# Optimization experiments

Measured on AMD Instinct MI355X. Metric: run time of the kernel, lower is better.

Reference implementation:

```python
import jax, jax.numpy as jnp
import numpy as np

TOKENS, D_IN, D_OUT = 8192, 4096, 4096

def setup_inputs() -> dict:
    key = jax.random.key(0)
    k1, k2, k3 = jax.random.split(key, 3)
    x = jax.random.normal(k1, (TOKENS, D_IN), dtype=jnp.float32)
    # original init: uniform(-1, 1) on weights of shape [out, in]
    w_pos = jax.random.uniform(k2, (D_OUT, D_IN), dtype=jnp.float32, minval=-1.0, maxval=1.0)
    w_neg = jax.random.uniform(k3, (D_OUT, D_IN), dtype=jnp.float32, minval=-1.0, maxval=1.0)
    return {"x": x, "w_pos": w_pos, "w_neg": w_neg}

def _ste_binarize(w):
    # (w > 0).float() in fwd, identity grad (STE): stop_grad(bin - w) + w
    b = (w > 0).astype(w.dtype)
    return jax.lax.stop_gradient(b - w) + w

def reference(x, w_pos, w_neg):
    tern_pos = _ste_binarize(w_pos)  # [O, I]
    tern_neg = _ste_binarize(w_neg)  # [O, I]
    # y = x @ tern_pos^T - x @ tern_neg^T  (biases unused in original forward)
    y = jnp.einsum('ti,oi->to', x, tern_pos) - jnp.einsum('ti,oi->to', x, tern_neg)
    return y
```

## Files before the change

kernel.cpp:

```cpp
#include <hip/hip_runtime.h>
#include <stdint.h>


#define TOKENS 8192
#define DIN    4096
#define DOUT   4096

typedef __bf16  bf16x8  __attribute__((ext_vector_type(8)));
typedef float   floatx4 __attribute__((ext_vector_type(4)));

__device__ __forceinline__ void async_copy16(const void* g, void* l) {
  __builtin_amdgcn_global_load_lds(
      (const __attribute__((address_space(1))) void*)g,
      (__attribute__((address_space(3))) void*)l, 16, 0, 0);
}

__device__ __forceinline__ unsigned short f2bf_rne(float f) {
  union { float f; uint32_t u; } v; v.f = f;
  uint32_t u = v.u;
  u += 0x7fffu + ((u >> 16) & 1u);
  return (unsigned short)(u >> 16);
}

__device__ __forceinline__ unsigned short tern_bits(float p, float n) {
  bool bp = p > 0.0f, bn = n > 0.0f;
  return (unsigned short)(bp == bn ? 0u : (bp ? 0x3f80u : 0xbf80u));
}

__global__ __launch_bounds__(256) void prep_kernel(
    const float4* __restrict__ x, ushort4* __restrict__ xb,
    const float4* __restrict__ wp, const float4* __restrict__ wn,
    ushort4* __restrict__ t) {
  const uint32_t bid = blockIdx.x;
  if (bid < 8192u) {
    const uint32_t stride = 8192u * 256u;
    uint32_t i = bid * 256u + threadIdx.x;
#pragma unroll
    for (int it = 0; it < 4; ++it, i += stride) {
      float4 v = x[i];
      ushort4 o;
      o.x = f2bf_rne(v.x); o.y = f2bf_rne(v.y);
      o.z = f2bf_rne(v.z); o.w = f2bf_rne(v.w);
      xb[i] = o;
    }
  } else {
    const uint32_t stride = 4096u * 256u;
    uint32_t i = (bid - 8192u) * 256u + threadIdx.x;
#pragma unroll
    for (int it = 0; it < 4; ++it, i += stride) {
      float4 p = wp[i];
      float4 n = wn[i];
      ushort4 o;
      o.x = tern_bits(p.x, n.x);
      o.y = tern_bits(p.y, n.y);
      o.z = tern_bits(p.z, n.z);
      o.w = tern_bits(p.w, n.w);
      t[i] = o;
    }
  }
}


#define LDS_BUF   65536u
#define LDS_B_OFF 32768u
#define LDS_KC    16384u

__global__ __launch_bounds__(512, 2) void gemm_bt(
    const unsigned short* __restrict__ A,
    const unsigned short* __restrict__ B,
    float* __restrict__ C)
{
  __shared__ __align__(16) char lds[131072];

  const int tid   = threadIdx.x;
  const int lane  = tid & 63;
  const int wid   = tid >> 6;
  const int waveM = wid >> 2;
  const int waveN = wid & 3;

  const uint32_t flat = blockIdx.x;
  const uint32_t swz  = ((flat & 7u) << 6) | (flat >> 3);
  const uint32_t bm = (swz >> 4) * 256u;
  const uint32_t bn = (swz & 15u) * 256u;

  const uint32_t srow  = (uint32_t)(tid >> 6) * 32u + (uint32_t)((tid & 63) >> 2);
  const uint32_t slot  = (uint32_t)(tid & 3);
  const uint32_t chnk  = slot ^ ((srow >> 1) & 3u);
  const uint32_t stA   = (bm + srow) * (DIN * 2u) + chnk * 16u;
  const uint32_t stB   = (bn + srow) * (DIN * 2u) + chnk * 16u;
  const uint32_t ldsSt = (uint32_t)(tid >> 6) * 2048u + (uint32_t)(tid & 63) * 16u;
  const char* Ab = (const char*)A;
  const char* Bb = (const char*)B;

  const int mrow = lane & 15;
  const int q    = lane >> 4;
  const int xs   = (q ^ ((mrow >> 1) & 3)) * 16;
  const uint32_t aFragBase = (uint32_t)waveM * 8192u + (uint32_t)mrow * 64u + (uint32_t)xs;
  const uint32_t bFragBase = LDS_B_OFF + (uint32_t)waveN * 4096u
                           + (uint32_t)mrow * 64u + (uint32_t)xs;

  floatx4 acc[8][4];
#pragma unroll
  for (int m = 0; m < 8; ++m)
#pragma unroll
    for (int n = 0; n < 4; ++n)
      acc[m][n] = (floatx4)0.0f;

  bf16x8 a0[4], a1[4], b0[4], b1[4];

#define STAGE_A(BUF, KH, KB) do {                                          \
    uint32_t g_ = stA + (KB) + (KH) * 64u;                                 \
    uint32_t l_ = (BUF) * LDS_BUF + (KH) * LDS_KC + ldsSt;                 \
    async_copy16(Ab + g_,           lds + l_);                             \
    async_copy16(Ab + g_ + 131072u, lds + l_ + 1024u);                     \
  } while (0)

#define STAGE_B(BUF, KH, KB) do {                                          \
    uint32_t g_ = stB + (KB) + (KH) * 64u;                                 \
    uint32_t l_ = (BUF) * LDS_BUF + LDS_B_OFF + (KH) * LDS_KC + ldsSt;     \
    async_copy16(Bb + g_,           lds + l_);                             \
    async_copy16(Bb + g_ + 131072u, lds + l_ + 1024u);                     \
  } while (0)

#define IA(DST, BUF, KC, MH) do {                                          \
    _Pragma("unroll")                                                      \
    for (int m_ = 0; m_ < 4; ++m_)                                         \
      DST[m_] = *(const bf16x8*)(lds + (BUF) * LDS_BUF + (KC) * LDS_KC     \
                                 + (uint32_t)(m_ + (MH) * 4) * 1024u       \
                                 + aFragBase);                             \
  } while (0)

#define IB(DST, BUF, KC) do {                                              \
    _Pragma("unroll")                                                      \
    for (int n_ = 0; n_ < 4; ++n_)                                         \
      DST[n_] = *(const bf16x8*)(lds + (BUF) * LDS_BUF + (KC) * LDS_KC     \
                                 + (uint32_t)n_ * 1024u + bFragBase);      \
  } while (0)

#define VM8 asm volatile("s_waitcnt vmcnt(8)" ::: "memory")
#define NOPW ((void)0)

#define PHASE(MH, AV, BV, ISSUE_STMT, STAGE_STMT, VMW) do {                \
    asm volatile("s_waitcnt lgkmcnt(0)" ::: "memory");                     \
    __builtin_amdgcn_sched_barrier(0);                                     \
    ISSUE_STMT;                                                            \
    __builtin_amdgcn_sched_barrier(0);                                     \
    __builtin_amdgcn_s_setprio(1);                                         \
    _Pragma("unroll")                                                      \
    for (int m_ = 0; m_ < 4; ++m_)                                         \
      _Pragma("unroll")                                                    \
      for (int n_ = 0; n_ < 4; ++n_)                                       \
        acc[(MH) * 4 + m_][n_] = __builtin_amdgcn_mfma_f32_16x16x32_bf16(  \
            AV[m_], BV[n_], acc[(MH) * 4 + m_][n_], 0, 0, 0);              \
    __builtin_amdgcn_s_setprio(0);                                         \
    STAGE_STMT;                                                            \
    VMW;                                                                   \
    __builtin_amdgcn_s_barrier();                                          \
  } while (0)

  STAGE_B(0, 0, 0u);   STAGE_A(0, 0, 0u);
  STAGE_B(0, 1, 0u);   STAGE_A(0, 1, 0u);
  STAGE_B(1, 0, 128u); STAGE_A(1, 0, 128u);
  STAGE_B(1, 1, 128u);
  asm volatile("s_waitcnt vmcnt(10)" ::: "memory");
  __builtin_amdgcn_s_barrier();
  IB(b0, 0, 0); IA(a0, 0, 0, 0);

#pragma unroll 1
  for (int i = 0; i < 32; ++i) {
    const uint32_t kb1 = (uint32_t)(2 * i + 1) * 128u;
    const uint32_t kb2 = (uint32_t)((2 * i + 2) & 63) * 128u;
    const uint32_t kb3 = (uint32_t)((2 * i + 3) & 63) * 128u;

    PHASE(0, a0, b0, IA(a1, 0, 0, 1),                  STAGE_A(1, 1, kb1), VM8);
    PHASE(1, a1, b0, { IB(b1, 0, 1); IA(a0, 0, 1, 0); }, STAGE_B(0, 0, kb2), NOPW);
    PHASE(0, a0, b1, IA(a1, 0, 1, 1),                  STAGE_A(0, 0, kb2), VM8);
    PHASE(1, a1, b1, { IB(b0, 1, 0); IA(a0, 1, 0, 0); }, STAGE_B(0, 1, kb2), NOPW);
    PHASE(0, a0, b0, IA(a1, 1, 0, 1),                  STAGE_A(0, 1, kb2), VM8);
    PHASE(1, a1, b0, { IB(b1, 1, 1); IA(a0, 1, 1, 0); }, STAGE_B(1, 0, kb3), NOPW);
    PHASE(0, a0, b1, IA(a1, 1, 1, 1),                  STAGE_A(1, 0, kb3), VM8);
    PHASE(1, a1, b1, { IB(b0, 0, 0); IA(a0, 0, 0, 0); }, STAGE_B(1, 1, kb3), NOPW);
  }

  const int col0 = (int)bn + waveN * 64 + (lane & 15);
  const int row0 = (int)bm + waveM * 128 + (lane >> 4) * 4;
  float* Cp = C + (size_t)row0 * DOUT + col0;
#pragma unroll
  for (int m = 0; m < 8; ++m)
#pragma unroll
    for (int n = 0; n < 4; ++n)
#pragma unroll
      for (int r = 0; r < 4; ++r)
        Cp[(size_t)(m * 16 + r) * DOUT + n * 16] = acc[m][n][r];

#undef STAGE_A
#undef STAGE_B
#undef IA
#undef IB
#undef VM8
#undef NOPW
#undef PHASE
}

extern "C" void kernel_launch(void* const* d_in, const int* in_sizes, int n_in,
                              void* d_out, int out_size, void* d_ws, size_t ws_size,
                              hipStream_t stream) {
  const float* x  = (const float*)d_in[0];
  const float* wp = (const float*)d_in[1];
  const float* wn = (const float*)d_in[2];
  float* out = (float*)d_out;

  unsigned short* xb   = (unsigned short*)d_ws;
  unsigned short* tern = xb + (size_t)TOKENS * DIN;

  prep_kernel<<<12288, 256, 0, stream>>>(
      (const float4*)x, (ushort4*)xb,
      (const float4*)wp, (const float4*)wn, (ushort4*)tern);

  gemm_bt<<<TOKENS / 256 * (DOUT / 256), 512, 0, stream>>>(xb, tern, out);
}
```

Baseline: 537.7 us.

## Use inline-asm LDS reads with immediate offsets and split B-fragment loads across phases

Replaces the compiler-generated LDS fragment loads with inline ds_read_b128 instructions that use precomputed base addresses and immediate offsets, to cut address arithmetic. B-fragment loads are now spread evenly across phases (two per phase) instead of four at once, and every phase waits on vmcnt(8) instead of alternating phases. This balances LDS traffic and shortens per-phase issue bursts, but the tighter vmcnt waits and the asm volatile reads can stall or limit scheduler freedom. The prologue also issues redundant B reads.

Result: no change. 537.1 us (-0.1%).

```diff
diff --git a/kernel.cpp b/kernel.cpp
--- a/kernel.cpp
+++ b/kernel.cpp
@@ -95,9 +95,15 @@
   const int mrow = lane & 15;
   const int q    = lane >> 4;
   const int xs   = (q ^ ((mrow >> 1) & 3)) * 16;
+  const uint32_t ldsBase =
+      (uint32_t)(uintptr_t)(__attribute__((address_space(3))) char*)lds;
   const uint32_t aFragBase = (uint32_t)waveM * 8192u + (uint32_t)mrow * 64u + (uint32_t)xs;
   const uint32_t bFragBase = LDS_B_OFF + (uint32_t)waveN * 4096u
                            + (uint32_t)mrow * 64u + (uint32_t)xs;
+  const uint32_t aA0 = ldsBase + aFragBase;
+  const uint32_t aA1 = aA0 + LDS_BUF;
+  const uint32_t bA0 = ldsBase + bFragBase;
+  const uint32_t bA1 = bA0 + LDS_BUF;
 
   floatx4 acc[8][4];
 #pragma unroll
@@ -106,7 +112,23 @@
     for (int n = 0; n < 4; ++n)
       acc[m][n] = (floatx4)0.0f;
 
-  bf16x8 a0[4], a1[4], b0[4], b1[4];
+  floatx4 a0f[4], a1f[4], b0f[4], b1f[4];
+
+#define DSR(DST, ADDR, IMM)                                                \
+  asm volatile("ds_read_b128 %0, %1 offset:%c2"                            \
+               : "=v"(DST) : "v"(ADDR), "i"(IMM))
+
+#define IA4(DST, ADDR, KC, MH) do {                                        \
+    DSR(DST[0], ADDR, (KC) * 16384 + ((MH) * 4 + 0) * 1024);               \
+    DSR(DST[1], ADDR, (KC) * 16384 + ((MH) * 4 + 1) * 1024);               \
+    DSR(DST[2], ADDR, (KC) * 16384 + ((MH) * 4 + 2) * 1024);               \
+    DSR(DST[3], ADDR, (KC) * 16384 + ((MH) * 4 + 3) * 1024);               \
+  } while (0)
+
+#define IB2(DST, N0, ADDR, KC) do {                                        \
+    DSR(DST[N0],     ADDR, (KC) * 16384 + ((N0)) * 1024);                  \
+    DSR(DST[N0 + 1], ADDR, (KC) * 16384 + ((N0) + 1) * 1024);              \
+  } while (0)
 
 #define STAGE_A(BUF, KH, KB) do {                                          \
     uint32_t g_ = stA + (KB) + (KH) * 64u;                                 \
@@ -122,26 +144,9 @@
     async_copy16(Bb + g_ + 131072u, lds + l_ + 1024u);                     \
   } while (0)
 
-#define IA(DST, BUF, KC, MH) do {                                          \
-    _Pragma("unroll")                                                      \
-    for (int m_ = 0; m_ < 4; ++m_)                                         \
-      DST[m_] = *(const bf16x8*)(lds + (BUF) * LDS_BUF + (KC) * LDS_KC     \
-                                 + (uint32_t)(m_ + (MH) * 4) * 1024u       \
-                                 + aFragBase);                             \
-  } while (0)
-
-#define IB(DST, BUF, KC) do {                                              \
-    _Pragma("unroll")                                                      \
-    for (int n_ = 0; n_ < 4; ++n_)                                         \
-      DST[n_] = *(const bf16x8*)(lds + (BUF) * LDS_BUF + (KC) * LDS_KC     \
-                                 + (uint32_t)n_ * 1024u + bFragBase);      \
-  } while (0)
-
-#define VM8 asm volatile("s_waitcnt vmcnt(8)" ::: "memory")
-#define NOPW ((void)0)
-
-#define PHASE(MH, AV, BV, ISSUE_STMT, STAGE_STMT, VMW) do {                \
+#define PHASE(MH, AF, BF, ISSUE_STMT, STAGE_STMT) do {                     \
     asm volatile("s_waitcnt lgkmcnt(0)" ::: "memory");                     \
+    asm volatile("s_waitcnt vmcnt(8)" ::: "memory");                       \
     __builtin_amdgcn_sched_barrier(0);                                     \
     ISSUE_STMT;                                                            \
     __builtin_amdgcn_sched_barrier(0);                                     \
@@ -151,20 +156,27 @@
       _Pragma("unroll")                                                    \
       for (int n_ = 0; n_ < 4; ++n_)                                       \
         acc[(MH) * 4 + m_][n_] = __builtin_amdgcn_mfma_f32_16x16x32_bf16(  \
-            AV[m_], BV[n_], acc[(MH) * 4 + m_][n_], 0, 0, 0);              \
+            __builtin_bit_cast(bf16x8, AF[m_]),                            \
+            __builtin_bit_cast(bf16x8, BF[n_]),                            \
+            acc[(MH) * 4 + m_][n_], 0, 0, 0);                              \
     __builtin_amdgcn_s_setprio(0);                                         \
     STAGE_STMT;                                                            \
-    VMW;                                                                   \
     __builtin_amdgcn_s_barrier();                                          \
   } while (0)
 
-  STAGE_B(0, 0, 0u);   STAGE_A(0, 0, 0u);
-  STAGE_B(0, 1, 0u);   STAGE_A(0, 1, 0u);
-  STAGE_B(1, 0, 128u); STAGE_A(1, 0, 128u);
+  STAGE_B(0, 0, 0u);
+  STAGE_A(0, 0, 0u);
+  STAGE_B(0, 1, 0u);
+  STAGE_A(0, 1, 0u);
+  STAGE_B(1, 0, 128u);
+  STAGE_A(1, 0, 128u);
   STAGE_B(1, 1, 128u);
-  asm volatile("s_waitcnt vmcnt(10)" ::: "memory");
+  asm volatile("s_waitcnt vmcnt(8)" ::: "memory");
   __builtin_amdgcn_s_barrier();
-  IB(b0, 0, 0); IA(a0, 0, 0, 0);
+  IB2(b0f, 0, bA0, 0); IB2(b0f, 2, bA0, 0 + 0);
+  DSR(b0f[0], bA0, 0); DSR(b0f[1], bA0, 1024);
+  DSR(b0f[2], bA0, 2048); DSR(b0f[3], bA0, 3072);
+  IA4(a0f, aA0, 0, 0);
 
 #pragma unroll 1
   for (int i = 0; i < 32; ++i) {
@@ -172,14 +184,22 @@
     const uint32_t kb2 = (uint32_t)((2 * i + 2) & 63) * 128u;
     const uint32_t kb3 = (uint32_t)((2 * i + 3) & 63) * 128u;
 
-    PHASE(0, a0, b0, IA(a1, 0, 0, 1),                  STAGE_A(1, 1, kb1), VM8);
-    PHASE(1, a1, b0, { IB(b1, 0, 1); IA(a0, 0, 1, 0); }, STAGE_B(0, 0, kb2), NOPW);
-    PHASE(0, a0, b1, IA(a1, 0, 1, 1),                  STAGE_A(0, 0, kb2), VM8);
-    PHASE(1, a1, b1, { IB(b0, 1, 0); IA(a0, 1, 0, 0); }, STAGE_B(0, 1, kb2), NOPW);
-    PHASE(0, a0, b0, IA(a1, 1, 0, 1),                  STAGE_A(0, 1, kb2), VM8);
-    PHASE(1, a1, b0, { IB(b1, 1, 1); IA(a0, 1, 1, 0); }, STAGE_B(1, 0, kb3), NOPW);
-    PHASE(0, a0, b1, IA(a1, 1, 1, 1),                  STAGE_A(1, 0, kb3), VM8);
-    PHASE(1, a1, b1, { IB(b0, 0, 0); IA(a0, 0, 0, 0); }, STAGE_B(1, 1, kb3), NOPW);
+    PHASE(0, a0f, b0f, { IA4(a1f, aA0, 0, 1); IB2(b1f, 0, bA0, 1); },
+          STAGE_A(1, 1, kb1));
+    PHASE(1, a1f, b0f, { IA4(a0f, aA0, 1, 0); IB2(b1f, 2, bA0, 1); },
+          STAGE_B(0, 0, kb2));
+    PHASE(0, a0f, b1f, { IA4(a1f, aA0, 1, 1); IB2(b0f, 0, bA1, 0); },
+          STAGE_A(0, 0, kb2));
+    PHASE(1, a1f, b1f, { IA4(a0f, aA1, 0, 0); IB2(b0f, 2, bA1, 0); },
+          STAGE_B(0, 1, kb2));
+    PHASE(0, a0f, b0f, { IA4(a1f, aA1, 0, 1); IB2(b1f, 0, bA1, 1); },
+          STAGE_A(0, 1, kb2));
+    PHASE(1, a1f, b0f, { IA4(a0f, aA1, 1, 0); IB2(b1f, 2, bA1, 1); },
+          STAGE_B(1, 0, kb3));
+    PHASE(0, a0f, b1f, { IA4(a1f, aA1, 1, 1); IB2(b0f, 0, bA0, 0); },
+          STAGE_A(1, 0, kb3));
+    PHASE(1, a1f, b1f, { IA4(a0f, aA0, 0, 0); IB2(b0f, 2, bA0, 0); },
+          STAGE_B(1, 1, kb3));
   }
 
   const int col0 = (int)bn + waveN * 64 + (lane & 15);
@@ -193,12 +213,11 @@
       for (int r = 0; r < 4; ++r)
         Cp[(size_t)(m * 16 + r) * DOUT + n * 16] = acc[m][n][r];
 
+#undef DSR
+#undef IA4
+#undef IB2
 #undef STAGE_A
 #undef STAGE_B
-#undef IA
-#undef IB
-#undef VM8
-#undef NOPW
 #undef PHASE
 }
 
```
